# Optimization experiments

Measured on AMD Instinct MI355X. Metric: run time of the kernel, lower is better.

Reference implementation:

```python
import jax, jax.numpy as jnp
import numpy as np
import math

N = 100000
E = 3200000
NFEAT = 128
NHID = 256
NCLASS = 16


def _uniform(key, shape, stdv):
    return jax.random.uniform(key, shape, jnp.float32, -stdv, stdv)


def setup_inputs() -> dict:
    key = jax.random.key(0)
    ks = jax.random.split(key, 16)
    x = jax.random.normal(ks[0], (N, NFEAT), jnp.float32)
    adj_row = jax.random.randint(ks[1], (E,), 0, N, jnp.int32)
    adj_col = jax.random.randint(ks[2], (E,), 0, N, jnp.int32)
    adj_val = jax.random.uniform(ks[3], (E,), jnp.float32)

    def gc_params(kw, kb, fin, fout):
        stdv = 1.0 / math.sqrt(fout)
        return _uniform(kw, (fin, fout), stdv), _uniform(kb, (fout,), stdv)

    w1, b1 = gc_params(ks[4], ks[5], NFEAT, NHID)
    w2, b2 = gc_params(ks[6], ks[7], NHID, NHID)
    w3, b3 = gc_params(ks[8], ks[9], NHID, NHID)
    w4, b4 = gc_params(ks[10], ks[11], NHID, NHID)
    fc_stdv = 1.0 / math.sqrt(NHID)
    fc_w = _uniform(ks[12], (NHID, NCLASS), fc_stdv)
    fc_b = _uniform(ks[13], (NCLASS,), fc_stdv)
    return {
        "x": x, "adj_val": adj_val,
        "w1": w1, "b1": b1, "w2": w2, "b2": b2,
        "w3": w3, "b3": b3, "w4": w4, "b4": b4,
        "fc_w": fc_w, "fc_b": fc_b,
        "adj_row": adj_row, "adj_col": adj_col,
    }


def _spmm(row, col, val, dense):
    # (sparse [N,N]) @ dense[N,D]: gather source rows, weight, scatter-add to dest
    msgs = dense[col] * val[:, None]  # [E, D]
    return jax.ops.segment_sum(msgs, row, num_segments=N)


def _gc_layer(x, row, col, val, w, b):
    support = x @ w              # dense GEMM [N, fout]
    out = _spmm(row, col, val, support)
    return out + b


def reference(x, adj_val, w1, b1, w2, b2, w3, b3, w4, b4, fc_w, fc_b, adj_row, adj_col):
    h = jax.nn.relu(_gc_layer(x, adj_row, adj_col, adj_val, w1, b1))
    h = jax.nn.relu(_gc_layer(h, adj_row, adj_col, adj_val, w2, b2))
    h = jax.nn.relu(_gc_layer(h, adj_row, adj_col, adj_val, w3, b3))
    h = jax.nn.relu(_gc_layer(h, adj_row, adj_col, adj_val, w4, b4))
    logits = h @ fc_w + fc_b
    return jax.nn.log_softmax(logits, axis=1)
```

## Files before the change

### kernel.cpp

```cpp
#include <hip/hip_runtime.h>
#include <hip/hip_bf16.h>

#define NN 100000
#define EE 3200000
#define NF 128
#define NH 256
#define NC 16
#define NB ((NN + 255) >> 8)
#define TILEA 8192
#define NBLKA ((EE + TILEA - 1) / TILEA)

typedef __bf16 bf16x8 __attribute__((ext_vector_type(8)));
typedef float f32x4 __attribute__((ext_vector_type(4)));
typedef float f32x2 __attribute__((ext_vector_type(2)));

static __device__ __forceinline__ unsigned short f2bf(float f) {
    unsigned int u = __builtin_bit_cast(unsigned int, f);
    u += 0x7FFFu + ((u >> 16) & 1u);
    return (unsigned short)(u >> 16);
}
static __device__ __forceinline__ float b2f(unsigned short h) {
    unsigned int u = ((unsigned int)h) << 16;
    return __builtin_bit_cast(float, u);
}
static __device__ __forceinline__ unsigned char f2fp8(float v) {
    return (unsigned char)(__builtin_amdgcn_cvt_pk_fp8_f32(v, v, 0, false) & 0xFF);
}

#define GLOAD_LDS16(g, l) __builtin_amdgcn_global_load_lds( \
    (const __attribute__((address_space(1))) unsigned int*)(g), \
    (__attribute__((address_space(3))) unsigned int*)(l), 16, 0, 0)

__global__ void k_cvt_fp8(const float* __restrict__ in, unsigned char* __restrict__ out, int n) {
    int i = (blockIdx.x * blockDim.x + threadIdx.x) * 4;
    if (i + 3 < n) {
        float4 v = *(const float4*)(in + i);
        int r = __builtin_amdgcn_cvt_pk_fp8_f32(v.x, v.y, 0, false);
        r = __builtin_amdgcn_cvt_pk_fp8_f32(v.z, v.w, r, true);
        *(unsigned int*)(out + i) = (unsigned int)r;
    } else {
        for (int t = 0; t < 4 && i + t < n; ++t) out[i + t] = f2fp8(in[i + t]);
    }
}

__global__ void k_wT4(const float* __restrict__ w1, const float* __restrict__ w2,
                      const float* __restrict__ w3, const float* __restrict__ w4,
                      unsigned short* __restrict__ Wt1, unsigned short* __restrict__ Wt2,
                      unsigned short* __restrict__ Wt3, unsigned short* __restrict__ Wt4) {
    int i = blockIdx.x * blockDim.x + threadIdx.x;
    if (i < NF * NH) {
        int k = i / NH, c = i % NH;
        Wt1[c * NF + k] = f2bf(w1[i]);
        return;
    }
    i -= NF * NH;
    int seg = i >> 16;
    int j = i & 65535;
    const float* W = (seg == 0) ? w2 : (seg == 1) ? w3 : w4;
    unsigned short* Wt = (seg == 0) ? Wt2 : (seg == 1) ? Wt3 : Wt4;
    int k = j >> 8, c = j & 255;
    Wt[c * NH + k] = f2bf(W[j]);
}

__global__ __launch_bounds__(256) void k_cnt(const int* __restrict__ row, int* __restrict__ cmat, int e) {
    __shared__ int hist[NB];
    int tid = threadIdx.x;
    int tile0 = blockIdx.x * TILEA;
    for (int b = tid; b < NB; b += 256) hist[b] = 0;
    __syncthreads();
#pragma unroll 8
    for (int t = 0; t < TILEA / 256; ++t) {
        int i = tile0 + t * 256 + tid;
        if (i < e) atomicAdd(&hist[row[i] >> 8], 1);
    }
    __syncthreads();
    for (int b = tid; b < NB; b += 256) cmat[b * NBLKA + blockIdx.x] = hist[b];
}

__global__ __launch_bounds__(512) void k_csum(int* __restrict__ cmat, int* __restrict__ btot) {
    __shared__ int lds[512];
    int b = blockIdx.x, tid = threadIdx.x;
    int v = (tid < NBLKA) ? cmat[b * NBLKA + tid] : 0;
    lds[tid] = v; __syncthreads();
    for (int off = 1; off < 512; off <<= 1) {
        int add = (tid >= off) ? lds[tid - off] : 0;
        __syncthreads();
        lds[tid] += add;
        __syncthreads();
    }
    if (tid < NBLKA) cmat[b * NBLKA + tid] = lds[tid] - v;
    if (tid == 511) btot[b] = lds[511];
}

__global__ __launch_bounds__(512) void k_bscan(const int* __restrict__ btot, int* __restrict__ bbase) {
    __shared__ int lds[512];
    int tid = threadIdx.x;
    int v = (tid < NB) ? btot[tid] : 0;
    lds[tid] = v; __syncthreads();
    for (int off = 1; off < 512; off <<= 1) {
        int add = (tid >= off) ? lds[tid - off] : 0;
        __syncthreads();
        lds[tid] += add;
        __syncthreads();
    }
    if (tid < NB) bbase[tid] = lds[tid] - v;
    if (tid == NB - 1) bbase[NB] = lds[tid];
}

__global__ __launch_bounds__(256) void k_scat2(const int* __restrict__ row, const int* __restrict__ col,
                                               const float* __restrict__ val, const int* __restrict__ cmat,
                                               const int* __restrict__ bbase,
                                               unsigned long long* __restrict__ tmp, int e) {
    __shared__ int hist[NB];
    __shared__ int base[NB];
    int tid = threadIdx.x;
    int tile0 = blockIdx.x * TILEA;
    for (int b = tid; b < NB; b += 256) {
        base[b] = bbase[b] + cmat[b * NBLKA + blockIdx.x];
        hist[b] = 0;
    }
    __syncthreads();
#pragma unroll 8
    for (int t = 0; t < TILEA / 256; ++t) {
        int i = tile0 + t * 256 + tid;
        if (i < e) {
            int r = row[i];
            int b = r >> 8;
            int rk = atomicAdd(&hist[b], 1);
            unsigned long long rec = ((unsigned long long)__builtin_bit_cast(unsigned int, val[i]) << 32)
                                   | (unsigned int)(col[i] | ((r & 255) << 17));
            tmp[base[b] + rk] = rec;
        }
    }
}

__global__ __launch_bounds__(256) void k_binB2(const int* __restrict__ bbase,
                                               const unsigned long long* __restrict__ tmp,
                                               unsigned int* __restrict__ pairs,
                                               int* __restrict__ rowp, int n) {
    __shared__ int hist[8192];
    __shared__ int part[256];
    int tid = threadIdx.x;
    int b = blockIdx.x;
    int r0 = b << 8;
    int s = bbase[b], e = bbase[b + 1];
    int base = tid * 32;
#pragma unroll
    for (int j = 0; j < 32; ++j) hist[base + j] = 0;
    __syncthreads();
    for (int i = s + tid; i < e; i += 256) {
        unsigned int w = (unsigned int)tmp[i];
        int key = (((w >> 17) & 255) << 5) | ((w & 0x1FFFFu) >> 12);
        atomicAdd(&hist[key], 1);
    }
    __syncthreads();
    int tot = 0;
#pragma unroll
    for (int j = 0; j < 32; ++j) { int x = hist[base + j]; hist[base + j] = tot; tot += x; }
    part[tid] = tot;
    __syncthreads();
    int v = tot;
    for (int off = 1; off < 256; off <<= 1) {
        int add = (tid >= off) ? part[tid - off] : 0;
        __syncthreads();
        part[tid] += add;
        __syncthreads();
    }
    int offex = part[tid] - v;
#pragma unroll
    for (int j = 0; j < 32; ++j) hist[base + j] += offex;
    __syncthreads();
    int rr = r0 + tid;
    if (rr < n) rowp[rr] = s + hist[tid << 5];
    if (b == 0 && tid == 0) rowp[n] = bbase[NB];
    __syncthreads();
    for (int i = s + tid; i < e; i += 256) {
        unsigned long long rec = tmp[i];
        unsigned int w = (unsigned int)rec;
        int key = (((w >> 17) & 255) << 5) | ((w & 0x1FFFFu) >> 12);
        unsigned int vb = (unsigned int)(rec >> 32);
        unsigned int bf = (vb + 0x7FFFu + ((vb >> 16) & 1u)) >> 16;
        unsigned int v15 = (bf + 1u) >> 1;
        int pos = s + atomicAdd(&hist[key], 1);
        pairs[pos] = (v15 << 17) | (w & 0x1FFFFu);
    }
}

template <bool BR, bool F8>
__global__ __launch_bounds__(256) void k_gemm(const unsigned short* __restrict__ A,
                                              const unsigned short* __restrict__ Bt,
                                              const float* __restrict__ bias,
                                              unsigned short* __restrict__ C,
                                              unsigned char* __restrict__ C8,
                                              int M, int K) {
    __shared__ unsigned short Atile[2][64 * 32];
    int tid = threadIdx.x;
    int wave = tid >> 6, lane = tid & 63;
    int row0 = blockIdx.x * 64;
    int colBase = wave * 64;
    int hr = lane & 15, kg = lane >> 4;

    int srow = tid >> 2;
    int selem = (tid & 3) * 8;
    int arow = row0 + srow; if (arow >= M) arow = M - 1;
    const unsigned short* srcBase = A + (size_t)arow * K + selem;

    f32x4 acc[4][4];
#pragma unroll
    for (int r = 0; r < 4; ++r)
#pragma unroll
        for (int c = 0; c < 4; ++c) acc[r][c] = (f32x4){0.f, 0.f, 0.f, 0.f};

    GLOAD_LDS16(srcBase, &Atile[0][0] + (size_t)tid * 8);
    __syncthreads();

    int cur = 0;
    for (int k0 = 0; k0 < K; k0 += 32) {
        if (k0 + 32 < K)
            GLOAD_LDS16(srcBase + k0 + 32, &Atile[cur ^ 1][0] + (size_t)tid * 8);
        bf16x8 af[4], bf_[4];
        int kk = k0 + kg * 8;
#pragma unroll
        for (int r = 0; r < 4; ++r)
            af[r] = *(const bf16x8*)(&Atile[cur][(r * 16 + hr) * 32 + kg * 8]);
#pragma unroll
        for (int c = 0; c < 4; ++c) {
            int bc = colBase + c * 16 + hr;
            bf_[c] = *(const bf16x8*)(Bt + (size_t)bc * K + kk);
        }
#pragma unroll
        for (int r = 0; r < 4; ++r)
#pragma unroll
            for (int c = 0; c < 4; ++c)
                acc[r][c] = __builtin_amdgcn_mfma_f32_16x16x32_bf16(af[r], bf_[c], acc[r][c], 0, 0, 0);
        __syncthreads();
        cur ^= 1;
    }
#pragma unroll
    for (int r = 0; r < 4; ++r)
#pragma unroll
        for (int c = 0; c < 4; ++c) {
            int col = colBase + c * 16 + hr;
            float bv = BR ? bias[col] : 0.f;
#pragma unroll
            for (int i = 0; i < 4; ++i) {
                int rr = row0 + r * 16 + kg * 4 + i;
                float v = acc[r][c][i];
                if (BR) v = fmaxf(v + bv, 0.f);
                if (rr < M) {
                    if (F8) C8[(size_t)rr * 256 + col] = f2fp8(v);
                    else    C[(size_t)rr * 256 + col] = f2bf(v);
                }
            }
        }
}

__global__ __launch_bounds__(256) void k_spmm256(const int* __restrict__ rowp,
                                                 const unsigned int* __restrict__ pairs,
                                                 const unsigned char* __restrict__ S,
                                                 const float* __restrict__ bias,
                                                 unsigned short* __restrict__ Hout, int n) {
    int lane = threadIdx.x & 63;
    int row = blockIdx.x * 4 + (threadIdx.x >> 6);
    if (row >= n) return;
    int s = rowp[row], e = rowp[row + 1];
    int half = lane >> 5;
    int f = (lane & 31) * 8;
    f32x2 a01 = {0.f, 0.f}, a23 = {0.f, 0.f}, a45 = {0.f, 0.f}, a67 = {0.f, 0.f};
#pragma unroll 4
    for (int i = s; i < e; i += 2) {
        int idx = i + half;
        bool act = idx < e;
        unsigned int p = pairs[act ? idx : i];
        unsigned int c = p & 0x1FFFFu;
        float v = __builtin_bit_cast(float, p & 0xFFFE0000u);
        if (!act) v = 0.f;
        uint2 t = *(const uint2*)(S + (size_t)c * 256 + f);
        f32x2 d0 = __builtin_amdgcn_cvt_pk_f32_fp8((int)t.x, false);
        f32x2 d1 = __builtin_amdgcn_cvt_pk_f32_fp8((int)t.x, true);
        f32x2 d2 = __builtin_amdgcn_cvt_pk_f32_fp8((int)t.y, false);
        f32x2 d3 = __builtin_amdgcn_cvt_pk_f32_fp8((int)t.y, true);
        a01 += d0 * v; a23 += d1 * v; a45 += d2 * v; a67 += d3 * v;
    }
    float a0 = a01.x + __shfl_xor(a01.x, 32);
    float a1 = a01.y + __shfl_xor(a01.y, 32);
    float a2 = a23.x + __shfl_xor(a23.x, 32);
    float a3 = a23.y + __shfl_xor(a23.y, 32);
    float a4 = a45.x + __shfl_xor(a45.x, 32);
    float a5 = a45.y + __shfl_xor(a45.y, 32);
    float a6 = a67.x + __shfl_xor(a67.x, 32);
    float a7 = a67.y + __shfl_xor(a67.y, 32);
    if (half == 0) {
        float4 b0 = *(const float4*)(bias + f);
        float4 b1 = *(const float4*)(bias + f + 4);
        a0 = fmaxf(a0 + b0.x, 0.f); a1 = fmaxf(a1 + b0.y, 0.f);
        a2 = fmaxf(a2 + b0.z, 0.f); a3 = fmaxf(a3 + b0.w, 0.f);
        a4 = fmaxf(a4 + b1.x, 0.f); a5 = fmaxf(a5 + b1.y, 0.f);
        a6 = fmaxf(a6 + b1.z, 0.f); a7 = fmaxf(a7 + b1.w, 0.f);
        uint4 o;
        o.x = (unsigned int)f2bf(a0) | ((unsigned int)f2bf(a1) << 16);
        o.y = (unsigned int)f2bf(a2) | ((unsigned int)f2bf(a3) << 16);
        o.z = (unsigned int)f2bf(a4) | ((unsigned int)f2bf(a5) << 16);
        o.w = (unsigned int)f2bf(a6) | ((unsigned int)f2bf(a7) << 16);
        *(uint4*)(Hout + (size_t)row * 256 + f) = o;
    }
}

__global__ __launch_bounds__(256) void k_spmm128(const int* __restrict__ rowp,
                                                 const unsigned int* __restrict__ pairs,
                                                 const unsigned char* __restrict__ X,
                                                 unsigned short* __restrict__ Out, int n) {
    int lane = threadIdx.x & 63;
    int row = blockIdx.x * 4 + (threadIdx.x >> 6);
    if (row >= n) return;
    int s = rowp[row], e = rowp[row + 1];
    int half = lane >> 5;
    int f = (lane & 31) * 4;
    f32x2 a01 = {0.f, 0.f}, a23 = {0.f, 0.f};
#pragma unroll 4
    for (int i = s; i < e; i += 2) {
        int idx = i + half;
        bool act = idx < e;
        unsigned int p = pairs[act ? idx : i];
        unsigned int c = p & 0x1FFFFu;
        float v = __builtin_bit_cast(float, p & 0xFFFE0000u);
        if (!act) v = 0.f;
        int w = *(const int*)(X + (size_t)c * 128 + f);
        f32x2 d0 = __builtin_amdgcn_cvt_pk_f32_fp8(w, false);
        f32x2 d1 = __builtin_amdgcn_cvt_pk_f32_fp8(w, true);
        a01 += d0 * v; a23 += d1 * v;
    }
    float a0 = a01.x + __shfl_xor(a01.x, 32);
    float a1 = a01.y + __shfl_xor(a01.y, 32);
    float a2 = a23.x + __shfl_xor(a23.x, 32);
    float a3 = a23.y + __shfl_xor(a23.y, 32);
    if (half == 0) {
        ushort4 o; o.x = f2bf(a0); o.y = f2bf(a1); o.z = f2bf(a2); o.w = f2bf(a3);
        *(ushort4*)(Out + (size_t)row * 128 + f) = o;
    }
}

__global__ __launch_bounds__(256) void k_fc_lsm(const unsigned short* __restrict__ H,
                                                const float* __restrict__ Wf,
                                                const float* __restrict__ bf,
                                                float* __restrict__ out, int n) {
    int lane = threadIdx.x & 63;
    int wave = threadIdx.x >> 6;
    int sub = lane >> 4, j = lane & 15;
    int node = (blockIdx.x * 4 + wave) * 4 + sub;
    bool valid = node < n;
    int nd = valid ? node : (n - 1);
    float acc = 0.f;
    for (int f0 = 0; f0 < NH; f0 += 8) {
        union { uint4 u; unsigned short s[8]; } h;
        h.u = *(const uint4*)(H + (size_t)nd * NH + f0);
#pragma unroll
        for (int t = 0; t < 8; ++t) acc += b2f(h.s[t]) * Wf[(f0 + t) * NC + j];
    }
    acc += bf[j];
    float mx = acc;
    for (int m = 1; m < 16; m <<= 1) mx = fmaxf(mx, __shfl_xor(mx, m, 16));
    float sm = __expf(acc - mx);
    for (int m = 1; m < 16; m <<= 1) sm += __shfl_xor(sm, m, 16);
    float res = acc - mx - __logf(sm);
    if (valid) out[(size_t)node * NC + j] = res;
}

extern "C" void kernel_launch(void* const* d_in, const int* in_sizes, int n_in,
                              void* d_out, int out_size, void* d_ws, size_t ws_size,
                              hipStream_t stream) {
    const float* x      = (const float*)d_in[0];
    const float* adjval = (const float*)d_in[1];
    const float* w1 = (const float*)d_in[2];  const float* b1 = (const float*)d_in[3];
    const float* w2 = (const float*)d_in[4];  const float* b2 = (const float*)d_in[5];
    const float* w3 = (const float*)d_in[6];  const float* b3 = (const float*)d_in[7];
    const float* w4 = (const float*)d_in[8];  const float* b4 = (const float*)d_in[9];
    const float* fcw = (const float*)d_in[10]; const float* fcb = (const float*)d_in[11];
    const int* arow = (const int*)d_in[12];
    const int* acol = (const int*)d_in[13];
    float* out = (float*)d_out;

    char* ws = (char*)d_ws;
    size_t off = 0;
    auto alloc = [&](size_t bytes) { size_t o = off; off += (bytes + 255) & ~(size_t)255; return o; };

    unsigned char*  xb  = (unsigned char*)(ws + alloc((size_t)NN * NF));
    unsigned short* Sb  = (unsigned short*)(ws + alloc((size_t)NN * NH * 2));
    unsigned short* H1  = (unsigned short*)(ws + alloc((size_t)NN * NH * 2));
    unsigned short* H2  = (unsigned short*)(ws + alloc((size_t)NN * NH * 2));
    unsigned short* Wt1 = (unsigned short*)(ws + alloc((size_t)NH * NF * 2));
    unsigned short* Wt2 = (unsigned short*)(ws + alloc((size_t)NH * NH * 2));
    unsigned short* Wt3 = (unsigned short*)(ws + alloc((size_t)NH * NH * 2));
    unsigned short* Wt4 = (unsigned short*)(ws + alloc((size_t)NH * NH * 2));
    int*   rowp   = (int*)(ws + alloc(((size_t)NN + 1) * 4));
    int*   cmat   = (int*)(ws + alloc((size_t)NB * NBLKA * 4));
    int*   btot   = (int*)(ws + alloc((size_t)NB * 4));
    int*   bbase  = (int*)(ws + alloc(((size_t)NB + 1) * 4));
    unsigned int* pairs = (unsigned int*)(ws + alloc((size_t)EE * 4));
    unsigned long long* tmp = (unsigned long long*)H2;
    unsigned char* S8 = (unsigned char*)Sb;

    k_cvt_fp8<<<(NN * NF / 4 + 255) / 256, 256, 0, stream>>>(x, xb, NN * NF);
    k_wT4<<<(NF * NH + 3 * NH * NH) / 256, 256, 0, stream>>>(w1, w2, w3, w4, Wt1, Wt2, Wt3, Wt4);

    k_cnt<<<NBLKA, 256, 0, stream>>>(arow, cmat, EE);
    k_csum<<<NB, 512, 0, stream>>>(cmat, btot);
    k_bscan<<<1, 512, 0, stream>>>(btot, bbase);
    k_scat2<<<NBLKA, 256, 0, stream>>>(arow, acol, adjval, cmat, bbase, tmp, EE);
    k_binB2<<<NB, 256, 0, stream>>>(bbase, tmp, pairs, rowp, NN);

    int gGemm = (NN + 63) / 64;
    int gSpmm = (NN + 3) / 4;
    k_spmm128<<<gSpmm, 256, 0, stream>>>(rowp, pairs, xb, Sb, NN);
    k_gemm<true, false><<<gGemm, 256, 0, stream>>>(Sb, Wt1, b1, H1, nullptr, NN, NF);
    k_gemm<false, true><<<gGemm, 256, 0, stream>>>(H1, Wt2, nullptr, nullptr, S8, NN, NH);
    k_spmm256<<<gSpmm, 256, 0, stream>>>(rowp, pairs, S8, b2, H2, NN);
    k_gemm<false, true><<<gGemm, 256, 0, stream>>>(H2, Wt3, nullptr, nullptr, S8, NN, NH);
    k_spmm256<<<gSpmm, 256, 0, stream>>>(rowp, pairs, S8, b3, H1, NN);
    k_gemm<false, true><<<gGemm, 256, 0, stream>>>(H1, Wt4, nullptr, nullptr, S8, NN, NH);
    k_spmm256<<<gSpmm, 256, 0, stream>>>(rowp, pairs, S8, b4, H2, NN);
    k_fc_lsm<<<(NN + 15) / 16, 256, 0, stream>>>(H2, fcw, fcb, out, NN);
}
```

Measured before the change: 879.8 us.

## Split spmm256 feature dimension into 8 column slices per row block

The 256-wide SpMM kernel now launches 8 blocks per row group, each handling a 32-byte feature slice. Within a wave, 8 edge groups each process every eighth edge and load 4 fp8 values per lane, and a shuffle tree reduces across the groups. The aim is more parallelism and more edges in flight per wave, to hide gather latency on rows with many edges. In exchange, each edge's pair index is read 8 times instead of once, and the gathered loads shrink to 4 bytes per lane.

Result: slower. 1.894 ms (+115.3%).

```diff
diff --git a/kernel.cpp b/kernel.cpp
--- a/kernel.cpp
+++ b/kernel.cpp
@@ -260,49 +260,37 @@
                                                  const unsigned char* __restrict__ S,
                                                  const float* __restrict__ bias,
                                                  unsigned short* __restrict__ Hout, int n) {
+    int slice = blockIdx.x & 7;
+    int rb = blockIdx.x >> 3;
+    int row = rb * 4 + (threadIdx.x >> 6);
+    if (row >= n) return;
     int lane = threadIdx.x & 63;
-    int row = blockIdx.x * 4 + (threadIdx.x >> 6);
-    if (row >= n) return;
+    int eg = lane >> 3;
+    int fl = lane & 7;
+    int f = slice * 32 + fl * 4;
     int s = rowp[row], e = rowp[row + 1];
-    int half = lane >> 5;
-    int f = (lane & 31) * 8;
-    f32x2 a01 = {0.f, 0.f}, a23 = {0.f, 0.f}, a45 = {0.f, 0.f}, a67 = {0.f, 0.f};
-#pragma unroll 4
-    for (int i = s; i < e; i += 2) {
-        int idx = i + half;
-        bool act = idx < e;
-        unsigned int p = pairs[act ? idx : i];
+    f32x2 a01 = {0.f, 0.f}, a23 = {0.f, 0.f};
+    for (int i = s + eg; i < e; i += 8) {
+        unsigned int p = pairs[i];
         unsigned int c = p & 0x1FFFFu;
         float v = __builtin_bit_cast(float, p & 0xFFFE0000u);
-        if (!act) v = 0.f;
-        uint2 t = *(const uint2*)(S + (size_t)c * 256 + f);
-        f32x2 d0 = __builtin_amdgcn_cvt_pk_f32_fp8((int)t.x, false);
-        f32x2 d1 = __builtin_amdgcn_cvt_pk_f32_fp8((int)t.x, true);
-        f32x2 d2 = __builtin_amdgcn_cvt_pk_f32_fp8((int)t.y, false);
-        f32x2 d3 = __builtin_amdgcn_cvt_pk_f32_fp8((int)t.y, true);
-        a01 += d0 * v; a23 += d1 * v; a45 += d2 * v; a67 += d3 * v;
-    }
-    float a0 = a01.x + __shfl_xor(a01.x, 32);
-    float a1 = a01.y + __shfl_xor(a01.y, 32);
-    float a2 = a23.x + __shfl_xor(a23.x, 32);
-    float a3 = a23.y + __shfl_xor(a23.y, 32);
-    float a4 = a45.x + __shfl_xor(a45.x, 32);
-    float a5 = a45.y + __shfl_xor(a45.y, 32);
-    float a6 = a67.x + __shfl_xor(a67.x, 32);
-    float a7 = a67.y + __shfl_xor(a67.y, 32);
-    if (half == 0) {
-        float4 b0 = *(const float4*)(bias + f);
-        float4 b1 = *(const float4*)(bias + f + 4);
-        a0 = fmaxf(a0 + b0.x, 0.f); a1 = fmaxf(a1 + b0.y, 0.f);
-        a2 = fmaxf(a2 + b0.z, 0.f); a3 = fmaxf(a3 + b0.w, 0.f);
-        a4 = fmaxf(a4 + b1.x, 0.f); a5 = fmaxf(a5 + b1.y, 0.f);
-        a6 = fmaxf(a6 + b1.z, 0.f); a7 = fmaxf(a7 + b1.w, 0.f);
-        uint4 o;
-        o.x = (unsigned int)f2bf(a0) | ((unsigned int)f2bf(a1) << 16);
-        o.y = (unsigned int)f2bf(a2) | ((unsigned int)f2bf(a3) << 16);
-        o.z = (unsigned int)f2bf(a4) | ((unsigned int)f2bf(a5) << 16);
-        o.w = (unsigned int)f2bf(a6) | ((unsigned int)f2bf(a7) << 16);
-        *(uint4*)(Hout + (size_t)row * 256 + f) = o;
+        int w = *(const int*)(S + (size_t)c * 256 + f);
+        f32x2 d0 = __builtin_amdgcn_cvt_pk_f32_fp8(w, false);
+        f32x2 d1 = __builtin_amdgcn_cvt_pk_f32_fp8(w, true);
+        a01 += d0 * v; a23 += d1 * v;
+    }
+    float a0 = a01.x, a1 = a01.y, a2 = a23.x, a3 = a23.y;
+#pragma unroll
+    for (int m = 8; m <= 32; m <<= 1) {
+        a0 += __shfl_xor(a0, m); a1 += __shfl_xor(a1, m);
+        a2 += __shfl_xor(a2, m); a3 += __shfl_xor(a3, m);
+    }
+    if (eg == 0) {
+        float4 bv = *(const float4*)(bias + f);
+        a0 = fmaxf(a0 + bv.x, 0.f); a1 = fmaxf(a1 + bv.y, 0.f);
+        a2 = fmaxf(a2 + bv.z, 0.f); a3 = fmaxf(a3 + bv.w, 0.f);
+        ushort4 o; o.x = f2bf(a0); o.y = f2bf(a1); o.z = f2bf(a2); o.w = f2bf(a3);
+        *(ushort4*)(Hout + (size_t)row * 256 + f) = o;
     }
 }
 
@@ -411,13 +399,14 @@
 
     int gGemm = (NN + 63) / 64;
     int gSpmm = (NN + 3) / 4;
+    int gSpmmS = gSpmm * 8;
     k_spmm128<<<gSpmm, 256, 0, stream>>>(rowp, pairs, xb, Sb, NN);
     k_gemm<true, false><<<gGemm, 256, 0, stream>>>(Sb, Wt1, b1, H1, nullptr, NN, NF);
     k_gemm<false, true><<<gGemm, 256, 0, stream>>>(H1, Wt2, nullptr, nullptr, S8, NN, NH);
-    k_spmm256<<<gSpmm, 256, 0, stream>>>(rowp, pairs, S8, b2, H2, NN);
+    k_spmm256<<<gSpmmS, 256, 0, stream>>>(rowp, pairs, S8, b2, H2, NN);
     k_gemm<false, true><<<gGemm, 256, 0, stream>>>(H2, Wt3, nullptr, nullptr, S8, NN, NH);
-    k_spmm256<<<gSpmm, 256, 0, stream>>>(rowp, pairs, S8, b3, H1, NN);
+    k_spmm256<<<gSpmmS, 256, 0, stream>>>(rowp, pairs, S8, b3, H1, NN);
     k_gemm<false, true><<<gGemm, 256, 0, stream>>>(H1, Wt4, nullptr, nullptr, S8, NN, NH);
-    k_spmm256<<<gSpmm, 256, 0, stream>>>(rowp, pairs, S8, b4, H2, NN);
+    k_spmm256<<<gSpmmS, 256, 0, stream>>>(rowp, pairs, S8, b4, H2, NN);
     k_fc_lsm<<<(NN + 15) / 16, 256, 0, stream>>>(H2, fcw, fcb, out, NN);
 }
```
